# Kernel optimization log

Measured on AMD Instinct MI355X. Metric: run time of the kernel, lower is better.

## Reference

```python
import jax, jax.numpy as jnp
import numpy as np

N_NODES = 50000
N_EDGES = 800000
F_IN = 128
HID = 128
F_ADD = 32
N_GRAPHS = 128


def setup_inputs() -> dict:
    key = jax.random.key(0)
    ks = jax.random.split(key, 12)
    x = jax.random.normal(ks[0], (N_NODES, F_IN), dtype=jnp.float32)
    edge_index = jax.random.randint(ks[1], (2, N_EDGES), 0, N_NODES, dtype=jnp.int64)
    batch = jnp.sort(jax.random.randint(ks[2], (N_NODES,), 0, N_GRAPHS, dtype=jnp.int64))
    additional_features = jax.random.normal(ks[3], (N_GRAPHS, F_ADD), dtype=jnp.float32)
    def glorot(k, shape):
        fan_in, fan_out = shape[0], shape[1]
        lim = jnp.sqrt(6.0 / (fan_in + fan_out)).astype(jnp.float32)
        return jax.random.uniform(k, shape, jnp.float32, -lim, lim)
    W1 = glorot(ks[4], (F_IN, HID)); b1 = jnp.zeros((HID,), jnp.float32)
    W2 = glorot(ks[5], (HID, HID)); b2 = jnp.zeros((HID,), jnp.float32)
    fc1_w = glorot(ks[6], (HID + F_ADD, HID)); fc1_b = jnp.zeros((HID,), jnp.float32)
    fc2_w = glorot(ks[7], (HID, 2)); fc2_b = jnp.zeros((2,), jnp.float32)
    return {"x": x, "edge_index": edge_index, "batch": batch,
            "additional_features": additional_features,
            "W1": W1, "b1": b1, "W2": W2, "b2": b2,
            "fc1_w": fc1_w, "fc1_b": fc1_b, "fc2_w": fc2_w, "fc2_b": fc2_b}


def _gcn_conv(h, src, dst, norm, W, b):
    # h: [N, d_in]; symmetric-normalized scatter-add aggregation (PyG GCNConv)
    h = h @ W                                   # [N, d_out]
    msg = h[src] * norm[:, None]                # gather + scale: [E+N, d_out]
    return jax.ops.segment_sum(msg, dst, num_segments=N_NODES) + b


def reference(x, edge_index, batch, additional_features,
              W1, b1, W2, b2, fc1_w, fc1_b, fc2_w, fc2_b):
    loops = jnp.arange(N_NODES, dtype=edge_index.dtype)
    src = jnp.concatenate([edge_index[0], loops])   # A + I
    dst = jnp.concatenate([edge_index[1], loops])
    deg = jax.ops.segment_sum(jnp.ones_like(src, dtype=x.dtype), dst,
                              num_segments=N_NODES)
    dinv = jnp.where(deg > 0, jax.lax.rsqrt(jnp.maximum(deg, 1.0)), 0.0)
    norm = dinv[src] * dinv[dst]

    h = jax.nn.relu(_gcn_conv(x, src, dst, norm, W1, b1))
    h = jax.nn.relu(_gcn_conv(h, src, dst, norm, W2, b2))
    # dropout is identity in eval mode

    sums = jax.ops.segment_sum(h, batch, num_segments=N_GRAPHS)    # [G, HID]
    counts = jax.ops.segment_sum(jnp.ones((N_NODES,), h.dtype), batch,
                                 num_segments=N_GRAPHS)
    pooled = sums / jnp.maximum(counts, 1.0)[:, None]              # global_mean_pool

    z = jnp.concatenate([pooled, additional_features], axis=1)     # [G, HID+F_ADD]
    z = jax.nn.relu(z @ fc1_w + fc1_b)
    return z @ fc2_w + fc2_b                                       # [G, 2]
```

## Files before the change

kernel.cpp:

```cpp
#include <hip/hip_runtime.h>

#define NN 50000
#define NE 800000
#define FD 128
#define FDH 64
#define FA 32
#define NG 128
#define EETOT (NE + NN)
#define NBLK ((NN + 255) / 256)
#define FEPB 2048
#define FNCH ((EETOT + FEPB - 1) / FEPB)
#define FILLB (FNCH * 8)
#define GEMMB ((NN + 63) / 64)
#define NPXCD 6250

typedef __attribute__((ext_vector_type(8))) short short8;
typedef __attribute__((ext_vector_type(4))) float f32x4;

__device__ __forceinline__ float bfbits(unsigned short u) {
    return __uint_as_float(((unsigned int)u) << 16);
}
__device__ __forceinline__ float bflo(unsigned int p) { return __uint_as_float(p << 16); }
__device__ __forceinline__ float bfhi(unsigned int p) { return __uint_as_float(p & 0xffff0000u); }
__device__ __forceinline__ unsigned short f2bf(float f) {
    unsigned int u = __float_as_uint(f);
    unsigned int r = u + 0x7FFFu + ((u >> 16) & 1u);
    return (unsigned short)(r >> 16);
}
__device__ __forceinline__ unsigned int packbf(float a, float b) {
    return (unsigned int)f2bf(a) | ((unsigned int)f2bf(b) << 16);
}

__device__ __forceinline__ int wave_probe_bf16(const unsigned int* t, int nwords) {
    int lane = threadIdx.x & 63;
    unsigned int wv = (lane < nwords) ? t[lane] : 0u;
    int nzp = (wv != 0u) ? 1 : 0;
    unsigned int e = (wv >> 7) & 0xFFu;
    int hitp = (nzp && e >= 100u && e <= 140u) ? 1 : 0;
    int nz = __popcll(__ballot(nzp));
    int hits = __popcll(__ballot(hitp));
    return (nz < 8) ? 1 : (hits * 4 >= nz * 3);
}
__device__ __forceinline__ int wave_probe_is64(const int* ei) {
    int lane = threadIdx.x & 63;
    int v = (lane < 32) ? ei[2 * lane + 1] : 0;
    return (__ballot(v != 0) == 0ull) ? 1 : 0;
}

__global__ __launch_bounds__(128) void mark_kernel(float* out, float v) {
    out[threadIdx.x] = v;
}

__global__ __launch_bounds__(256) void prep(
        const void* addf, const void* w1, const void* b1, const void* w2,
        const void* b2, const void* fc1w, const void* fc1b, const void* fc2w,
        const void* fc2b, unsigned int* W1t, unsigned int* W2t,
        float* addff, float* b1f, float* b2f, float* fc1wf, float* fc1bf,
        float* fc2wf, float* fc2bf, int* degi, int* tsum) {
    int b = blockIdx.x;
    if (b < 64) {
        int rel = b * 256 + threadIdx.x;
        const void* src = (rel < 8192) ? w1 : w2;
        unsigned int* dst = (rel < 8192) ? W1t : W2t;
        int flag = wave_probe_bf16((const unsigned int*)src, 64);
        int rr = rel & 8191;
        int n = rr >> 6, kk = rr & 63;
        float lo, hi;
        if (flag) {
            const unsigned short* s = (const unsigned short*)src;
            lo = bfbits(s[(2 * kk) * FD + n]);
            hi = bfbits(s[(2 * kk + 1) * FD + n]);
        } else {
            const float* s = (const float*)src;
            lo = s[(2 * kk) * FD + n];
            hi = s[(2 * kk + 1) * FD + n];
        }
        dst[rr] = packbf(lo, hi);
    } else if (b < 163) {
        int i = (b - 64) * 256 + threadIdx.x;
        int wb = (b - 64) * 256 + (threadIdx.x & ~63);
        const void* src; float* dst; int base; int prnw; int lim;
        if      (wb < 4096)  { src = addf; dst = addff; base = 0;     prnw = 64; lim = 4096;  }
        else if (wb < 4224)  { src = b1;   dst = b1f;   base = 4096;  prnw = 64; lim = 128;   }
        else if (wb < 4352)  { src = b2;   dst = b2f;   base = 4224;  prnw = 64; lim = 128;   }
        else if (wb < 24832) { src = fc1w; dst = fc1wf; base = 4352;  prnw = 64; lim = 20480; }
        else if (wb < 24960) { src = fc1b; dst = fc1bf; base = 24832; prnw = 64; lim = 128;   }
        else if (wb < 25216) { src = fc2w; dst = fc2wf; base = 24960; prnw = 64; lim = 256;   }
        else if (wb < 25280) { src = fc2b; dst = fc2bf; base = 25216; prnw = 1;  lim = 2;     }
        else return;
        int flag = wave_probe_bf16((const unsigned int*)src, prnw);
        int rel = i - base;
        if (rel < lim) {
            if (flag) dst[rel] = bfbits(((const unsigned short*)src)[rel]);
            else      dst[rel] = ((const float*)src)[rel];
        }
    } else {
        int i = (b - 163) * 256 + threadIdx.x;
        if      (i < NN)       degi[i] = 0;
        else if (i < NN + 256) tsum[i - NN] = 0;
    }
}

__global__ __launch_bounds__(256) void deg_kernel(const int* ei, int* deg,
                                                  int* s32, int* d32) {
    int is64 = wave_probe_is64(ei);
    int e = blockIdx.x * 256 + threadIdx.x;
    if (e < NE) {
        int s = is64 ? ei[2 * e] : ei[e];
        int d = is64 ? ei[2 * (NE + e)] : ei[NE + e];
        s32[e] = s;
        d32[e] = d;
        atomicAdd(&deg[d], 1);
    }
}

__global__ __launch_bounds__(256) void scan_fused(const int* degi, const int* batch,
        int* tsum, float* dinv, int* rowstart, int* cursor, int* gstart) {
    __shared__ int sh[256];
    int b = blockIdx.x, t = threadIdx.x;
    int i = b * 256 + t;
    int d = (i < NN) ? degi[i] : 0;
    if (i < NN) dinv[i] = rsqrtf((float)(d + 1));
    int v = (i < NN) ? d + 1 : 0;
    sh[t] = v;
    __syncthreads();
    for (int off = 1; off < 256; off <<= 1) {
        int a = (t >= off) ? sh[t - off] : 0;
        __syncthreads();
        sh[t] += a;
        __syncthreads();
    }
    int incl = sh[t];
    int total = sh[255];
    if (t == 0) atomicExch(&tsum[b], total);
    int pt = 0;
    for (int j = t; j < b; j += 256) {
        int s;
        do { s = atomicAdd(&tsum[j], 0); } while (s == 0);
        pt += s;
    }
    __syncthreads();
    sh[t] = pt;
    __syncthreads();
    for (int off = 128; off >= 1; off >>= 1) {
        if (t < off) sh[t] += sh[t + off];
        __syncthreads();
    }
    int boff = sh[0];
    if (i < NN) {
        int r = boff + incl - v;
        rowstart[i] = r;
        cursor[i]   = r;
    }
    if (i == 0) rowstart[NN] = EETOT;
    if (i < NN) {
        int is64 = (batch[NN - 1] == 0) ? 1 : 0;
        int bc = is64 ? batch[2 * i] : batch[i];
        if (i == 0) {
            for (int g = 0; g <= bc; ++g) gstart[g] = 0;
        } else {
            int bp = is64 ? batch[2 * (i - 1)] : batch[i - 1];
            for (int g = bp + 1; g <= bc; ++g) gstart[g] = i;
        }
        if (i == NN - 1) {
            for (int g = bc + 1; g <= NG; ++g) gstart[g] = NN;
        }
    }
}

__global__ __launch_bounds__(256) void fill_gemm(const int* s32, const int* d32,
        const float* dinv, int* cursor, unsigned int* cv,
        const void* __restrict__ Av, const unsigned int* __restrict__ Wt,
        unsigned short* __restrict__ C) {
    if ((int)blockIdx.x < FILLB) {
        int chunk = blockIdx.x >> 3;
        int par   = blockIdx.x & 7;
        int base  = chunk * FEPB;
        #pragma unroll
        for (int k = 0; k < FEPB / 256; ++k) {
            int e = base + k * 256 + threadIdx.x;
            if (e >= EETOT) break;
            int s, d;
            if (e < NE) { d = d32[e]; s = -1; }
            else        { s = d = e - NE; }
            if (d / NPXCD != par) continue;
            if (s < 0) s = s32[e];
            int pos = atomicAdd(&cursor[d], 1);
            cv[pos] = (unsigned int)s | ((unsigned int)f2bf(dinv[s] * dinv[d]) << 16);
        }
        return;
    }
    int bid = blockIdx.x - FILLB;
    int wave = threadIdx.x >> 6;
    int lane = threadIdx.x & 63;
    int quad = lane >> 4;
    int l16  = lane & 15;
    int mbase = bid * 64 + wave * 16;
    int ra = mbase + l16;
    if (ra >= NN) ra = NN - 1;
    bool f32in = !wave_probe_bf16((const unsigned int*)Av, 64);
    short8 af[4];
    if (!f32in) {
        const uint4* Arow = (const uint4*)((const unsigned int*)Av + (size_t)ra * FDH);
        #pragma unroll
        for (int kk = 0; kk < 4; ++kk) {
            uint4 v = Arow[kk * 4 + quad];
            af[kk] = *(short8*)&v;
        }
    } else {
        const float* Arow = (const float*)Av + (size_t)ra * FD;
        #pragma unroll
        for (int kk = 0; kk < 4; ++kk) {
            const float4* p = (const float4*)(Arow + (kk * 4 + quad) * 8);
            float4 u = p[0], v = p[1];
            uint4 q;
            q.x = packbf(u.x, u.y); q.y = packbf(u.z, u.w);
            q.z = packbf(v.x, v.y); q.w = packbf(v.z, v.w);
            af[kk] = *(short8*)&q;
        }
    }
    #pragma unroll
    for (int nt = 0; nt < 8; ++nt) {
        int n = nt * 16 + l16;
        const uint4* Wrow = (const uint4*)(Wt + (size_t)n * FDH);
        f32x4 acc = {0.f, 0.f, 0.f, 0.f};
        #pragma unroll
        for (int kk = 0; kk < 4; ++kk) {
            uint4 wv = Wrow[kk * 4 + quad];
            short8 bf = *(short8*)&wv;
            acc = __builtin_amdgcn_mfma_f32_16x16x32_bf16(af[kk], bf, acc, 0, 0, 0);
        }
        int row0 = mbase + quad * 4;
        #pragma unroll
        for (int reg = 0; reg < 4; ++reg) {
            int r = row0 + reg;
            if (r < NN) C[(size_t)r * FD + nt * 16 + l16] = f2bf(acc[reg]);
        }
    }
}

__global__ __launch_bounds__(256) void gemm_mfma(const unsigned int* __restrict__ Av,
        const unsigned int* __restrict__ Wt, unsigned short* __restrict__ C) {
    int wave = threadIdx.x >> 6;
    int lane = threadIdx.x & 63;
    int quad = lane >> 4;
    int l16  = lane & 15;
    int mbase = blockIdx.x * 64 + wave * 16;
    int ra = mbase + l16;
    if (ra >= NN) ra = NN - 1;
    short8 af[4];
    const uint4* Arow = (const uint4*)(Av + (size_t)ra * FDH);
    #pragma unroll
    for (int kk = 0; kk < 4; ++kk) {
        uint4 v = Arow[kk * 4 + quad];
        af[kk] = *(short8*)&v;
    }
    #pragma unroll
    for (int nt = 0; nt < 8; ++nt) {
        int n = nt * 16 + l16;
        const uint4* Wrow = (const uint4*)(Wt + (size_t)n * FDH);
        f32x4 acc = {0.f, 0.f, 0.f, 0.f};
        #pragma unroll
        for (int kk = 0; kk < 4; ++kk) {
            uint4 wv = Wrow[kk * 4 + quad];
            short8 bf = *(short8*)&wv;
            acc = __builtin_amdgcn_mfma_f32_16x16x32_bf16(af[kk], bf, acc, 0, 0, 0);
        }
        int row0 = mbase + quad * 4;
        #pragma unroll
        for (int reg = 0; reg < 4; ++reg) {
            int r = row0 + reg;
            if (r < NN) C[(size_t)r * FD + nt * 16 + l16] = f2bf(acc[reg]);
        }
    }
}

__global__ __launch_bounds__(256) void aggregate_kernel(const unsigned int* Hb,
        const unsigned int* cv, const int* rowstart, const float* bias,
        unsigned int* outb) {
    int lane = threadIdx.x & 63;
    int r4   = lane >> 4;
    int c4   = lane & 15;
    int wv   = threadIdx.x >> 6;
    int n = blockIdx.x * 16 + wv * 4 + r4;
    const uint4* H4 = (const uint4*)Hb;
    int jb = rowstart[n], je = rowstart[n + 1];
    float a0 = 0.f, a1 = 0.f, a2 = 0.f, a3 = 0.f;
    float a4 = 0.f, a5 = 0.f, a6 = 0.f, a7 = 0.f;
    int j = jb;
    for (; j + 7 < je; j += 8) {
        unsigned int rr[8]; uint4 hh[8];
        #pragma unroll
        for (int k = 0; k < 8; ++k) rr[k] = cv[j + k];
        #pragma unroll
        for (int k = 0; k < 8; ++k) hh[k] = H4[(size_t)(rr[k] & 0xFFFFu) * 16 + c4];
        #pragma unroll
        for (int k = 0; k < 8; ++k) {
            float v = bfbits((unsigned short)(rr[k] >> 16));
            a0 += v * bflo(hh[k].x); a1 += v * bfhi(hh[k].x);
            a2 += v * bflo(hh[k].y); a3 += v * bfhi(hh[k].y);
            a4 += v * bflo(hh[k].z); a5 += v * bfhi(hh[k].z);
            a6 += v * bflo(hh[k].w); a7 += v * bfhi(hh[k].w);
        }
    }
    for (; j + 3 < je; j += 4) {
        unsigned int rr[4]; uint4 hh[4];
        #pragma unroll
        for (int k = 0; k < 4; ++k) rr[k] = cv[j + k];
        #pragma unroll
        for (int k = 0; k < 4; ++k) hh[k] = H4[(size_t)(rr[k] & 0xFFFFu) * 16 + c4];
        #pragma unroll
        for (int k = 0; k < 4; ++k) {
            float v = bfbits((unsigned short)(rr[k] >> 16));
            a0 += v * bflo(hh[k].x); a1 += v * bfhi(hh[k].x);
            a2 += v * bflo(hh[k].y); a3 += v * bfhi(hh[k].y);
            a4 += v * bflo(hh[k].z); a5 += v * bfhi(hh[k].z);
            a6 += v * bflo(hh[k].w); a7 += v * bfhi(hh[k].w);
        }
    }
    for (; j < je; ++j) {
        unsigned int r = cv[j];
        uint4 h = H4[(size_t)(r & 0xFFFFu) * 16 + c4];
        float v = bfbits((unsigned short)(r >> 16));
        a0 += v * bflo(h.x); a1 += v * bfhi(h.x);
        a2 += v * bflo(h.y); a3 += v * bfhi(h.y);
        a4 += v * bflo(h.z); a5 += v * bfhi(h.z);
        a6 += v * bflo(h.w); a7 += v * bfhi(h.w);
    }
    a0 = fmaxf(a0 + bias[8 * c4 + 0], 0.f);
    a1 = fmaxf(a1 + bias[8 * c4 + 1], 0.f);
    a2 = fmaxf(a2 + bias[8 * c4 + 2], 0.f);
    a3 = fmaxf(a3 + bias[8 * c4 + 3], 0.f);
    a4 = fmaxf(a4 + bias[8 * c4 + 4], 0.f);
    a5 = fmaxf(a5 + bias[8 * c4 + 5], 0.f);
    a6 = fmaxf(a6 + bias[8 * c4 + 6], 0.f);
    a7 = fmaxf(a7 + bias[8 * c4 + 7], 0.f);
    uint4 out;
    out.x = packbf(a0, a1);
    out.y = packbf(a2, a3);
    out.z = packbf(a4, a5);
    out.w = packbf(a6, a7);
    ((uint4*)outb)[(size_t)n * 16 + c4] = out;
}

__global__ __launch_bounds__(256) void poolhead(const unsigned int* Hb,
        const int* gstart, const float* addf, const float* fc1w, const float* fc1b,
        const float* fc2w, const float* fc2b, const unsigned int* x, void* outp) {
    int g = blockIdx.x;
    int t = threadIdx.x;
    int q = t >> 6, w = t & 63;
    int obf = wave_probe_bf16(x, 64);
    int s = gstart[g], e = gstart[g + 1];
    float a0 = 0.f, a1 = 0.f;
    #pragma unroll 4
    for (int n = s + q; n < e; n += 4) {
        unsigned int h = Hb[(size_t)n * FDH + w];
        a0 += bflo(h);
        a1 += bfhi(h);
    }
    __shared__ float pp[4][FD];
    __shared__ float z[FD + FA];
    __shared__ float h[FD];
    pp[q][2 * w]     = a0;
    pp[q][2 * w + 1] = a1;
    __syncthreads();
    if (t < FD) {
        float cnt = (float)(e - s);
        if (cnt < 1.0f) cnt = 1.0f;
        z[t] = (pp[0][t] + pp[1][t] + pp[2][t] + pp[3][t]) / cnt;
    }
    if (t >= FD && t < FD + FA) z[t] = addf[g * FA + (t - FD)];
    __syncthreads();
    if (t < FD) {
        float acc = fc1b[t];
        #pragma unroll 4
        for (int k = 0; k < FD + FA; ++k)
            acc += z[k] * fc1w[k * FD + t];
        h[t] = fmaxf(acc, 0.f);
    }
    __syncthreads();
    if (t < 2) {
        float o = fc2b[t];
        for (int j = 0; j < FD; ++j) o += h[j] * fc2w[j * 2 + t];
        if (obf) ((unsigned short*)outp)[g * 2 + t] = f2bf(o);
        else     ((float*)outp)[g * 2 + t] = o;
    }
}

extern "C" void kernel_launch(void* const* d_in, const int* in_sizes, int n_in,
                              void* d_out, int out_size, void* d_ws, size_t ws_size,
                              hipStream_t stream) {
    (void)out_size;

    if (n_in != 12) {
        hipLaunchKernelGGL(mark_kernel, dim3(1), dim3(128), 0, stream,
                           (float*)d_out, 2000.0f);
        return;
    }
    const int exp_sizes[12] = {6400000, 1600000, 50000, 4096, 16384, 128,
                               16384, 128, 20480, 128, 256, 2};
    for (int i = 0; i < 12; ++i) {
        if (in_sizes[i] != exp_sizes[i]) {
            hipLaunchKernelGGL(mark_kernel, dim3(1), dim3(128), 0, stream,
                               (float*)d_out, 3000.0f + 100.0f * i);
            return;
        }
    }

    size_t off = 0;
    char* base = (char*)d_ws;
#define WSALLOC(ptr, type, nbytes) \
    type* ptr = (type*)(base + off); off += (((size_t)(nbytes)) + 255) & ~(size_t)255;
    WSALLOC(bufA,  unsigned int, (size_t)NN * FDH * 4)
    WSALLOC(bufB,  unsigned int, (size_t)NN * FDH * 4)
    WSALLOC(dinv,  float, (size_t)NN * 4)
    WSALLOC(degi,  int,   (size_t)NN * 4)
    WSALLOC(rowst, int,   (size_t)(NN + 1) * 4)
    WSALLOC(cursor,int,   (size_t)NN * 4)
    WSALLOC(tsum,  int,   256 * 4)
    WSALLOC(cv,    unsigned int, (size_t)EETOT * 4)
    WSALLOC(gstart,int,   (size_t)(NG + 1) * 4)
    WSALLOC(s32,   int,   (size_t)NE * 4)
    WSALLOC(d32,   int,   (size_t)NE * 4)
    WSALLOC(W1t,   unsigned int, (size_t)FD * FDH * 4)
    WSALLOC(W2t,   unsigned int, (size_t)FD * FDH * 4)
    WSALLOC(b1f,   float, FD * 4)
    WSALLOC(b2f,   float, FD * 4)
    WSALLOC(addff, float, (size_t)NG * FA * 4)
    WSALLOC(fc1wf, float, (size_t)(FD + FA) * FD * 4)
    WSALLOC(fc1bf, float, FD * 4)
    WSALLOC(fc2wf, float, FD * 2 * 4)
    WSALLOC(fc2bf, float, 2 * 4)
#undef WSALLOC
    if (ws_size < off) {
        hipLaunchKernelGGL(mark_kernel, dim3(1), dim3(128), 0, stream,
                           (float*)d_out, 1000.0f);
        return;
    }

    const int* ei    = (const int*)d_in[1];
    const int* batch = (const int*)d_in[2];

    hipLaunchKernelGGL(prep, dim3(360), dim3(256), 0, stream,
                       d_in[3], d_in[4], d_in[5], d_in[6], d_in[7],
                       d_in[8], d_in[9], d_in[10], d_in[11],
                       W1t, W2t, addff, b1f, b2f, fc1wf, fc1bf,
                       fc2wf, fc2bf, degi, tsum);

    hipLaunchKernelGGL(deg_kernel, dim3((NE + 255) / 256), dim3(256), 0, stream,
                       ei, degi, s32, d32);
    hipLaunchKernelGGL(scan_fused, dim3(NBLK), dim3(256), 0, stream,
                       degi, batch, tsum, dinv, rowst, cursor, gstart);

    hipLaunchKernelGGL(fill_gemm, dim3(FILLB + GEMMB), dim3(256), 0, stream,
                       s32, d32, dinv, cursor, cv,
                       d_in[0], W1t, (unsigned short*)bufA);

    hipLaunchKernelGGL(aggregate_kernel, dim3(NN / 16), dim3(256), 0, stream,
                       bufA, cv, rowst, b1f, bufB);
    hipLaunchKernelGGL(gemm_mfma, dim3(GEMMB), dim3(256), 0, stream,
                       bufB, W2t, (unsigned short*)bufA);
    hipLaunchKernelGGL(aggregate_kernel, dim3(NN / 16), dim3(256), 0, stream,
                       bufA, cv, rowst, b2f, bufB);

    hipLaunchKernelGGL(poolhead, dim3(NG), dim3(256), 0, stream,
                       bufB, gstart, addff, fc1wf, fc1bf, fc2wf, fc2bf,
                       (const unsigned int*)d_in[0], d_out);
}
```

Measured before the change: 299.6 us.

## Pre-bin edges by destination partition during degree counting to shrink CSR fill

```diff
diff --git a/kernel.cpp b/kernel.cpp
--- a/kernel.cpp
+++ b/kernel.cpp
@@ -8,11 +8,12 @@
 #define NG 128
 #define EETOT (NE + NN)
 #define NBLK ((NN + 255) / 256)
-#define FEPB 2048
-#define FNCH ((EETOT + FEPB - 1) / FEPB)
-#define FILLB (FNCH * 8)
+#define NPXCD 6250
+#define ECHK 2048
+#define NCHK ((NE + ECHK - 1) / ECHK)
+#define FPB 52
+#define FILLB (8 * FPB)
 #define GEMMB ((NN + 63) / 64)
-#define NPXCD 6250
 
 typedef __attribute__((ext_vector_type(8))) short short8;
 typedef __attribute__((ext_vector_type(4))) float f32x4;
@@ -101,16 +102,48 @@
     }
 }
 
-__global__ __launch_bounds__(256) void deg_kernel(const int* ei, int* deg,
-                                                  int* s32, int* d32) {
+__global__ __launch_bounds__(256) void bin_kernel(const int* ei, int* deg,
+        int2* ebsd, int* bofs) {
+    __shared__ int cnt[8];
+    __shared__ int base[8];
     int is64 = wave_probe_is64(ei);
-    int e = blockIdx.x * 256 + threadIdx.x;
-    if (e < NE) {
-        int s = is64 ? ei[2 * e] : ei[e];
-        int d = is64 ? ei[2 * (NE + e)] : ei[NE + e];
-        s32[e] = s;
-        d32[e] = d;
-        atomicAdd(&deg[d], 1);
+    int chunk = blockIdx.x;
+    int e0 = chunk * ECHK;
+    int nedge = NE - e0; if (nedge > ECHK) nedge = ECHK;
+    if (threadIdx.x < 8) cnt[threadIdx.x] = 0;
+    __syncthreads();
+    int sA[8], dA[8], rk[8], pr[8];
+    #pragma unroll
+    for (int k = 0; k < 8; ++k) {
+        int j = k * 256 + threadIdx.x;
+        pr[k] = -1;
+        if (j < nedge) {
+            int e = e0 + j;
+            int s = is64 ? ei[2 * e] : ei[e];
+            int d = is64 ? ei[2 * (NE + e)] : ei[NE + e];
+            atomicAdd(&deg[d], 1);
+            int p = d / NPXCD;
+            sA[k] = s; dA[k] = d; pr[k] = p;
+            rk[k] = atomicAdd(&cnt[p], 1);
+        }
+    }
+    __syncthreads();
+    if (threadIdx.x == 0) {
+        int acc = 0;
+        #pragma unroll
+        for (int p = 0; p < 8; ++p) {
+            base[p] = acc;
+            bofs[chunk * 8 + p] = acc;
+            acc += cnt[p];
+        }
+    }
+    __syncthreads();
+    #pragma unroll
+    for (int k = 0; k < 8; ++k) {
+        if (pr[k] >= 0) {
+            int idx = chunk * ECHK + base[pr[k]] + rk[k];
+            ebsd[idx] = make_int2(sA[k], dA[k]);
+        }
     }
 }
 
@@ -168,25 +201,29 @@
     }
 }
 
-__global__ __launch_bounds__(256) void fill_gemm(const int* s32, const int* d32,
+__global__ __launch_bounds__(256) void fill_gemm(const int2* ebsd, const int* bofs,
         const float* dinv, int* cursor, unsigned int* cv,
         const void* __restrict__ Av, const unsigned int* __restrict__ Wt,
         unsigned short* __restrict__ C) {
     if ((int)blockIdx.x < FILLB) {
-        int chunk = blockIdx.x >> 3;
-        int par   = blockIdx.x & 7;
-        int base  = chunk * FEPB;
-        #pragma unroll
-        for (int k = 0; k < FEPB / 256; ++k) {
-            int e = base + k * 256 + threadIdx.x;
-            if (e >= EETOT) break;
-            int s, d;
-            if (e < NE) { d = d32[e]; s = -1; }
-            else        { s = d = e - NE; }
-            if (d / NPXCD != par) continue;
-            if (s < 0) s = s32[e];
-            int pos = atomicAdd(&cursor[d], 1);
-            cv[pos] = (unsigned int)s | ((unsigned int)f2bf(dinv[s] * dinv[d]) << 16);
+        int par = blockIdx.x & 7;
+        int g   = blockIdx.x >> 3;
+        for (int chunk = g; chunk < NCHK; chunk += FPB) {
+            int b0 = bofs[chunk * 8 + par];
+            int nedge = NE - chunk * ECHK; if (nedge > ECHK) nedge = ECHK;
+            int b1 = (par < 7) ? bofs[chunk * 8 + par + 1] : nedge;
+            for (int j = b0 + (int)threadIdx.x; j < b1; j += 256) {
+                int2 sd = ebsd[chunk * ECHK + j];
+                int pos = atomicAdd(&cursor[sd.y], 1);
+                cv[pos] = (unsigned int)sd.x
+                        | ((unsigned int)f2bf(dinv[sd.x] * dinv[sd.y]) << 16);
+            }
+        }
+        for (int n = par * NPXCD + g * 256 + threadIdx.x; n < (par + 1) * NPXCD;
+             n += FPB * 256) {
+            int pos = atomicAdd(&cursor[n], 1);
+            float di = dinv[n];
+            cv[pos] = (unsigned int)n | ((unsigned int)f2bf(di * di) << 16);
         }
         return;
     }
@@ -420,8 +457,8 @@
     WSALLOC(tsum,  int,   256 * 4)
     WSALLOC(cv,    unsigned int, (size_t)EETOT * 4)
     WSALLOC(gstart,int,   (size_t)(NG + 1) * 4)
-    WSALLOC(s32,   int,   (size_t)NE * 4)
-    WSALLOC(d32,   int,   (size_t)NE * 4)
+    WSALLOC(ebsd,  int2,  (size_t)NCHK * ECHK * 8)
+    WSALLOC(bofs,  int,   (size_t)NCHK * 8 * 4)
     WSALLOC(W1t,   unsigned int, (size_t)FD * FDH * 4)
     WSALLOC(W2t,   unsigned int, (size_t)FD * FDH * 4)
     WSALLOC(b1f,   float, FD * 4)
@@ -447,13 +484,13 @@
                        W1t, W2t, addff, b1f, b2f, fc1wf, fc1bf,
                        fc2wf, fc2bf, degi, tsum);
 
-    hipLaunchKernelGGL(deg_kernel, dim3((NE + 255) / 256), dim3(256), 0, stream,
-                       ei, degi, s32, d32);
+    hipLaunchKernelGGL(bin_kernel, dim3(NCHK), dim3(256), 0, stream,
+                       ei, degi, ebsd, bofs);
     hipLaunchKernelGGL(scan_fused, dim3(NBLK), dim3(256), 0, stream,
                        degi, batch, tsum, dinv, rowst, cursor, gstart);
 
     hipLaunchKernelGGL(fill_gemm, dim3(FILLB + GEMMB), dim3(256), 0, stream,
-                       s32, d32, dinv, cursor, cv,
+                       ebsd, bofs, dinv, cursor, cv,
                        d_in[0], W1t, (unsigned short*)bufA);
 
     hipLaunchKernelGGL(aggregate_kernel, dim3(NN / 16), dim3(256), 0, stream,
```

After: 287.2 us. -4.2%, faster.
